# Optimization experiments

Measured on AMD Instinct MI355X. Metric: run time of the kernel, lower is better.

Reference implementation:

```python
import jax, jax.numpy as jnp
import numpy as np


def setup_inputs() -> dict:
    key = jax.random.key(0)
    ks = jax.random.split(key, 8)
    dim, E = 128, 8
    b, t, h, w = 2, 16, 64, 64
    scale = 1.0 / np.sqrt(dim)
    return {
        "x": jax.random.normal(ks[0], (b, dim, t, h, w), jnp.float32),
        "gate_w": jax.random.normal(ks[1], (dim, E), jnp.float32) * scale,
        "gate_b": jax.random.normal(ks[2], (E,), jnp.float32) * 0.01,
        "W1": jax.random.normal(ks[3], (E, dim, dim), jnp.float32) * scale,
        "b1": jax.random.normal(ks[4], (E, dim), jnp.float32) * 0.01,
        "alpha": jnp.full((E,), 0.25, jnp.float32),  # PReLU default init
        "W2": jax.random.normal(ks[5], (E, dim, dim), jnp.float32) * scale,
        "b2": jax.random.normal(ks[6], (E, dim), jnp.float32) * 0.01,
        "top_k": 2,
    }


def reference(x, gate_w, gate_b, W1, b1, alpha, W2, b2, top_k):
    b, c, t, h, w = x.shape
    E = gate_w.shape[1]
    # tokens: [N, c] with N = b*t*h*w (matches permute(0,2,3,4,1).reshape(-1,c))
    xf = jnp.transpose(x, (0, 2, 3, 4, 1)).reshape(-1, c)
    N = xf.shape[0]
    logits = xf @ gate_w + gate_b                      # [N, E]
    vals, idx = jax.lax.top_k(logits, top_k)           # [N, K]
    probs = jax.nn.softmax(vals, axis=1)               # softmax over selected logits
    # scatter combine weights to dense [N, E] (zero for unselected experts)
    combine = jnp.zeros((N, E), xf.dtype).at[jnp.arange(N)[:, None], idx].add(probs)
    # expert MLP (1x1x1 conv == per-token linear), scalar PReLU per expert
    h1 = jnp.einsum('nc,eoc->eno', xf, W1) + b1[:, None, :]          # [E, N, c]
    h1 = jnp.maximum(h1, 0) + alpha[:, None, None] * jnp.minimum(h1, 0)
    h2 = jnp.einsum('eno,epo->enp', h1, W2) + b2[:, None, :]         # [E, N, c]
    out = jnp.einsum('ne,enc->nc', combine, h2)                      # weighted combine
    out = jnp.transpose(out.reshape(b, t, h, w, c), (0, 4, 1, 2, 3))
    return out + x
```

## Files before the change

kernel.cpp:

```cpp
#include <hip/hip_runtime.h>

typedef float f32x4  __attribute__((ext_vector_type(4)));
typedef float f32x16 __attribute__((ext_vector_type(16)));
typedef __bf16 bf16x8 __attribute__((ext_vector_type(8)));

#define SPAT 65536
#define CH   128
#define NE   8

#define SLOT(i)  ((i) * 32768)
#define B1_OFF   65536
#define B2T_OFF  69632
#define AL_OFF   73728
#define LDS_BYTES 73760

static __device__ __forceinline__ unsigned short bf(float f) {
    __bf16 h = (__bf16)f; return __builtin_bit_cast(unsigned short, h);
}
static __device__ __forceinline__ unsigned pk2(float a, float b) {
    return (unsigned)bf(a) | ((unsigned)bf(b) << 16);
}

typedef const __attribute__((address_space(1))) void* as1cp;
typedef __attribute__((address_space(3))) void* as3p;
static __device__ __forceinline__ void gload16(const void* g, void* l) {
    __builtin_amdgcn_global_load_lds((as1cp)g, (as3p)l, 16, 0, 0);
}

__global__ void conv_w(const float* __restrict__ W1, const float* __restrict__ W2,
                       unsigned char* __restrict__ wimg) {
    const int gid = blockIdx.x * 256 + threadIdx.x;
    const int mat = gid >> 14;
    const int e   = (gid >> 11) & 7;
    const int r   = (gid >> 4) & 127;
    const int p   = gid & 15;
    if (mat == 0) {
        const int sg = p ^ (r & 15);
        const int n = 4 * (r >> 5) + ((r >> 3) & 3);
        const int src_row = (n >> 1) * 16 + ((r >> 2) & 1) * 8 + (n & 1) * 4 + (r & 3);
        const float* s = W1 + (e * 16384 + src_row * 128 + sg * 8);
        uint4 pk;
        pk.x = pk2(s[0], s[1]); pk.y = pk2(s[2], s[3]);
        pk.z = pk2(s[4], s[5]); pk.w = pk2(s[6], s[7]);
        *(uint4*)(wimg + e * 32768 + r * 256 + p * 16) = pk;
    } else {
        const float* s = W2 + (e * 16384 + r * 128 + p * 8);
        uint4 pk;
        pk.x = pk2(s[0], s[1]); pk.y = pk2(s[2], s[3]);
        pk.z = pk2(s[4], s[5]); pk.w = pk2(s[6], s[7]);
        *(uint4*)(wimg + 262144 + e * 32768
                  + ((((p >> 1) * 4 + (r >> 5)) << 10) + ((p & 1) << 9) + (r & 31) * 16)) = pk;
    }
}

static __device__ __forceinline__ void stage_w32(const unsigned char* __restrict__ src,
                                                 unsigned char* dst, int t) {
    const int off = t * 16;
    gload16(src + off,          dst + off);
    gload16(src + 8192  + off,  dst + 8192  + off);
    gload16(src + 16384 + off,  dst + 16384 + off);
    gload16(src + 24576 + off,  dst + 24576 + off);
}

__global__ __launch_bounds__(512) __attribute__((amdgpu_waves_per_eu(2, 2)))
void moe_main(const float* __restrict__ x,  const float* __restrict__ gw,
              const float* __restrict__ gb, const float* __restrict__ b1,
              const float* __restrict__ alpha, const float* __restrict__ b2,
              const unsigned char* __restrict__ wimg, float* __restrict__ out)
{
    __shared__ __align__(16) unsigned char smem[LDS_BYTES];
    const int t = threadIdx.x, lane = t & 63, w = t >> 6, blk = blockIdx.x;
    const int ltok = lane & 31, hi = lane >> 5, l15 = lane & 15;
    const size_t xbase = (size_t)(blk >> 8) * (size_t)(CH * SPAT) + (size_t)((blk & 255) << 8);
    const int m = w * 32 + ltok;
    const int wlane = (hi << 9) + ltok * 16;

    stage_w32(wimg, smem + SLOT(0), t);

    if (t < 256) ((f32x4*)(smem + B1_OFF))[t] = ((const f32x4*)b1)[t];
    if (t < 128) {
        uint4 pkv, z4 = {0u, 0u, 0u, 0u};
        pkv.x = pk2(b2[0 * 128 + t], b2[1 * 128 + t]);
        pkv.y = pk2(b2[2 * 128 + t], b2[3 * 128 + t]);
        pkv.z = pk2(b2[4 * 128 + t], b2[5 * 128 + t]);
        pkv.w = pk2(b2[6 * 128 + t], b2[7 * 128 + t]);
        *(uint4*)(smem + B2T_OFF + t * 32)      = pkv;
        *(uint4*)(smem + B2T_OFF + t * 32 + 16) = z4;
    } else if (t >= 128 && t < 136) {
        ((float*)(smem + AL_OFF))[t - 128] = alpha[t - 128];
    }

    f32x4 plo = {0.f,0.f,0.f,0.f}, phi = {0.f,0.f,0.f,0.f};
    uint4 xb[8];
    #pragma unroll
    for (int kc = 0; kc < 8; ++kc) {
        const int c0 = kc * 16 + hi * 8;
        float v8[8];
        #pragma unroll
        for (int j = 0; j < 8; ++j) v8[j] = x[xbase + (size_t)(c0 + j) * SPAT + m];
        #pragma unroll
        for (int j = 0; j < 8; ++j) {
            const f32x4 g0 = *(const f32x4*)(gw + (c0 + j) * NE);
            const f32x4 g1 = *(const f32x4*)(gw + (c0 + j) * NE + 4);
            plo += v8[j] * g0; phi += v8[j] * g1;
        }
        xb[kc].x = pk2(v8[0], v8[1]); xb[kc].y = pk2(v8[2], v8[3]);
        xb[kc].z = pk2(v8[4], v8[5]); xb[kc].w = pk2(v8[6], v8[7]);
    }
    #pragma unroll
    for (int i2 = 0; i2 < 4; ++i2) {
        plo[i2] += __shfl_xor(plo[i2], 32, 64);
        phi[i2] += __shfl_xor(phi[i2], 32, 64);
    }
    int i0, i1; float q0, q1; uint4 cbw;
    {
        float lg[8];
        #pragma unroll
        for (int e2 = 0; e2 < 4; ++e2) { lg[e2] = plo[e2] + gb[e2]; lg[4 + e2] = phi[e2] + gb[4 + e2]; }
        i0 = 0; float v0 = lg[0];
        #pragma unroll
        for (int e2 = 1; e2 < 8; ++e2) if (lg[e2] > v0) { v0 = lg[e2]; i0 = e2; }
        i1 = -1; float v1 = -3.4e38f;
        #pragma unroll
        for (int e2 = 0; e2 < 8; ++e2) if (e2 != i0 && lg[e2] > v1) { v1 = lg[e2]; i1 = e2; }
        const float d = expf(v1 - v0);
        q0 = 1.f / (1.f + d);
        q1 = d   / (1.f + d);
        float cb[8];
        #pragma unroll
        for (int e2 = 0; e2 < 8; ++e2) cb[e2] = (e2 == i0) ? q0 : ((e2 == i1) ? q1 : 0.f);
        cbw.x = pk2(cb[0], cb[1]); cbw.y = pk2(cb[2], cb[3]);
        cbw.z = pk2(cb[4], cb[5]); cbw.w = pk2(cb[6], cb[7]);
    }
    __syncthreads();

    f32x16 acc[4] = {};

    #pragma unroll 1
    for (int e = 0; e < NE; ++e) {
        const int cur = e & 1;
        if (e < 7) stage_w32(wimg + (e + 1) * 32768, smem + SLOT(cur ^ 1), t);
        const unsigned char* WA  = smem + SLOT(cur);
        const unsigned char* W2g = wimg + 262144 + e * 32768;
        const float alph = ((const float*)(smem + AL_OFF))[e];
        const float ce = (i0 == e) ? q0 : ((i1 == e) ? q1 : 0.f);

        #pragma unroll 1
        for (int g = 0; g < 4; ++g) {
            uint4 a1[8];
            #pragma unroll
            for (int kc = 0; kc < 8; ++kc)
                a1[kc] = *(const uint4*)(WA + (g * 32 + ltok) * 256
                                          + (((kc * 2 + hi) ^ l15) * 16));
            f32x16 h0 = {}, h1 = {};
            #pragma unroll
            for (int kc = 0; kc < 4; ++kc) {
                h0 = __builtin_amdgcn_mfma_f32_32x32x16_bf16(
                        __builtin_bit_cast(bf16x8, a1[2 * kc]),
                        __builtin_bit_cast(bf16x8, xb[2 * kc]), h0, 0, 0, 0);
                h1 = __builtin_amdgcn_mfma_f32_32x32x16_bf16(
                        __builtin_bit_cast(bf16x8, a1[2 * kc + 1]),
                        __builtin_bit_cast(bf16x8, xb[2 * kc + 1]), h1, 0, 0, 0);
            }
            uint4 pa2[2];
            #pragma unroll
            for (int q = 0; q < 4; ++q) {
                const int n = 4 * g + q, kt2 = n >> 1, half = n & 1;
                const int obase = kt2 * 16 + hi * 8 + half * 4;
                const f32x4 b1v = *(const f32x4*)(smem + B1_OFF + e * 512 + obase * 4);
                float hv[4];
                #pragma unroll
                for (int i = 0; i < 4; ++i) {
                    float z = h0[q * 4 + i] + h1[q * 4 + i] + b1v[i];
                    z = (z > 0.f) ? z : alph * z;
                    hv[i] = z * ce;
                }
                ((unsigned*)&pa2[q >> 1])[half * 2]     = pk2(hv[0], hv[1]);
                ((unsigned*)&pa2[q >> 1])[half * 2 + 1] = pk2(hv[2], hv[3]);
            }
            #pragma unroll
            for (int dk = 0; dk < 2; ++dk) {
                const int kt2 = 2 * g + dk;
                #pragma unroll
                for (int n2 = 0; n2 < 4; ++n2) {
                    const uint4 wf = *(const uint4*)(W2g + ((kt2 * 4 + n2) << 10) + wlane);
                    acc[n2] = __builtin_amdgcn_mfma_f32_32x32x16_bf16(
                            __builtin_bit_cast(bf16x8, pa2[dk]),
                            __builtin_bit_cast(bf16x8, wf), acc[n2], 0, 0, 0);
                }
            }
        }
        __syncthreads();
    }

    {
        const uint4 z4 = {0u, 0u, 0u, 0u};
        const uint4 aop = hi ? z4 : cbw;
        #pragma unroll
        for (int n2 = 0; n2 < 4; ++n2) {
            const uint4 bop = *(const uint4*)(smem + B2T_OFF + (n2 * 32 + ltok) * 32 + hi * 16);
            acc[n2] = __builtin_amdgcn_mfma_f32_32x32x16_bf16(
                    __builtin_bit_cast(bf16x8, aop),
                    __builtin_bit_cast(bf16x8, bop), acc[n2], 0, 0, 0);
        }
    }

    #pragma unroll
    for (int n2 = 0; n2 < 4; ++n2) {
        const int p = n2 * 32 + ltok;
        #pragma unroll
        for (int q = 0; q < 4; ++q) {
            const int tok0 = w * 32 + q * 8 + hi * 4;
            const size_t a = xbase + (size_t)p * SPAT + tok0;
            const f32x4 xv = *(const f32x4*)(x + a);
            f32x4 r;
            #pragma unroll
            for (int i = 0; i < 4; ++i) r[i] = acc[n2][q * 4 + i] + xv[i];
            *(f32x4*)(out + a) = r;
        }
    }
}

extern "C" void kernel_launch(void* const* d_in, const int* in_sizes, int n_in,
                              void* d_out, int out_size, void* d_ws, size_t ws_size,
                              hipStream_t stream) {
    const float* x  = (const float*)d_in[0];
    const float* gw = (const float*)d_in[1];
    const float* gb = (const float*)d_in[2];
    const float* W1 = (const float*)d_in[3];
    const float* b1 = (const float*)d_in[4];
    const float* al = (const float*)d_in[5];
    const float* W2 = (const float*)d_in[6];
    const float* b2 = (const float*)d_in[7];
    (void)in_sizes; (void)n_in; (void)out_size; (void)ws_size;
    unsigned char* wimg = (unsigned char*)d_ws;
    float* out = (float*)d_out;

    conv_w<<<dim3(128), dim3(256), 0, stream>>>(W1, W2, wimg);
    moe_main<<<dim3(512), dim3(512), 0, stream>>>(x, gw, gb, b1, al, b2, wimg, out);
}
```

Baseline: 122.1 us.

## Load W1 fragments from global into registers with double buffering, drop LDS staging

W1 is no longer staged into LDS through global_load_lds. It is repacked into the same MFMA-fragment layout as W2 and loaded straight from global (L2) into registers. The loads are software-pipelined one (expert, group) iteration ahead, with sched_barriers to keep the order, which removes the per-expert __syncthreads and LDS reads. LDS use drops from about 72 KB to about 8 KB. In exchange the kernel carries more VGPRs for the two prefetch buffers and the W2 fragments, and every wave now pulls its weights from L2 instead of sharing them through LDS.

```diff
diff --git a/kernel.cpp b/kernel.cpp
--- a/kernel.cpp
+++ b/kernel.cpp
@@ -8,23 +8,18 @@
 #define CH   128
 #define NE   8
 
-#define SLOT(i)  ((i) * 32768)
-#define B1_OFF   65536
-#define B2T_OFF  69632
-#define AL_OFF   73728
-#define LDS_BYTES 73760
+#define B1_OFF   0
+#define B2T_OFF  4096
+#define AL_OFF   8192
+#define LDS_BYTES 8224
+
+#define SB() __builtin_amdgcn_sched_barrier(0)
 
 static __device__ __forceinline__ unsigned short bf(float f) {
     __bf16 h = (__bf16)f; return __builtin_bit_cast(unsigned short, h);
 }
 static __device__ __forceinline__ unsigned pk2(float a, float b) {
     return (unsigned)bf(a) | ((unsigned)bf(b) << 16);
-}
-
-typedef const __attribute__((address_space(1))) void* as1cp;
-typedef __attribute__((address_space(3))) void* as3p;
-static __device__ __forceinline__ void gload16(const void* g, void* l) {
-    __builtin_amdgcn_global_load_lds((as1cp)g, (as3p)l, 16, 0, 0);
 }
 
 __global__ void conv_w(const float* __restrict__ W1, const float* __restrict__ W2,
@@ -34,32 +29,84 @@
     const int e   = (gid >> 11) & 7;
     const int r   = (gid >> 4) & 127;
     const int p   = gid & 15;
+    int src_row = r;
     if (mat == 0) {
-        const int sg = p ^ (r & 15);
         const int n = 4 * (r >> 5) + ((r >> 3) & 3);
-        const int src_row = (n >> 1) * 16 + ((r >> 2) & 1) * 8 + (n & 1) * 4 + (r & 3);
-        const float* s = W1 + (e * 16384 + src_row * 128 + sg * 8);
-        uint4 pk;
-        pk.x = pk2(s[0], s[1]); pk.y = pk2(s[2], s[3]);
-        pk.z = pk2(s[4], s[5]); pk.w = pk2(s[6], s[7]);
-        *(uint4*)(wimg + e * 32768 + r * 256 + p * 16) = pk;
-    } else {
-        const float* s = W2 + (e * 16384 + r * 128 + p * 8);
-        uint4 pk;
-        pk.x = pk2(s[0], s[1]); pk.y = pk2(s[2], s[3]);
-        pk.z = pk2(s[4], s[5]); pk.w = pk2(s[6], s[7]);
-        *(uint4*)(wimg + 262144 + e * 32768
-                  + ((((p >> 1) * 4 + (r >> 5)) << 10) + ((p & 1) << 9) + (r & 31) * 16)) = pk;
-    }
-}
-
-static __device__ __forceinline__ void stage_w32(const unsigned char* __restrict__ src,
-                                                 unsigned char* dst, int t) {
-    const int off = t * 16;
-    gload16(src + off,          dst + off);
-    gload16(src + 8192  + off,  dst + 8192  + off);
-    gload16(src + 16384 + off,  dst + 16384 + off);
-    gload16(src + 24576 + off,  dst + 24576 + off);
+        src_row = (n >> 1) * 16 + ((r >> 2) & 1) * 8 + (n & 1) * 4 + (r & 3);
+    }
+    const float* s = (mat ? W2 : W1) + (e * 16384 + src_row * 128 + p * 8);
+    uint4 pk;
+    pk.x = pk2(s[0], s[1]); pk.y = pk2(s[2], s[3]);
+    pk.z = pk2(s[4], s[5]); pk.w = pk2(s[6], s[7]);
+    *(uint4*)(wimg + mat * 262144 + e * 32768
+              + ((((p >> 1) * 4 + (r >> 5)) << 10) + ((p & 1) << 9) + (r & 31) * 16)) = pk;
+}
+
+static __device__ __forceinline__ void ld_a1g(uint4* buf, const unsigned char* __restrict__ base,
+                                              int g, int wlane) {
+    #pragma unroll
+    for (int kc = 0; kc < 8; ++kc)
+        buf[kc] = *(const uint4*)(base + ((kc * 4 + g) << 10) + wlane);
+}
+
+static __device__ __forceinline__ void body(
+        int it, uint4* cur, uint4* nxt,
+        const unsigned char* __restrict__ wimg, const unsigned char* smem,
+        int wlane, int hi, int i0, int i1, float q0, float q1,
+        const uint4* xb, f32x16* acc)
+{
+    const int e = it >> 2, g = it & 3;
+    const unsigned char* W2g = wimg + 262144 + e * 32768;
+
+    uint4 wfb[8];
+    #pragma unroll
+    for (int dk = 0; dk < 2; ++dk)
+        #pragma unroll
+        for (int n2 = 0; n2 < 4; ++n2)
+            wfb[dk * 4 + n2] = *(const uint4*)(W2g + (((2 * g + dk) * 4 + n2) << 10) + wlane);
+    SB();
+    if (it < 31) {
+        const int en = (it + 1) >> 2, gn = (it + 1) & 3;
+        ld_a1g(nxt, wimg + en * 32768, gn, wlane);
+    }
+    SB();
+
+    f32x16 h0 = {}, h1 = {};
+    #pragma unroll
+    for (int kc = 0; kc < 4; ++kc) {
+        h0 = __builtin_amdgcn_mfma_f32_32x32x16_bf16(
+                __builtin_bit_cast(bf16x8, cur[2 * kc]),
+                __builtin_bit_cast(bf16x8, xb[2 * kc]), h0, 0, 0, 0);
+        h1 = __builtin_amdgcn_mfma_f32_32x32x16_bf16(
+                __builtin_bit_cast(bf16x8, cur[2 * kc + 1]),
+                __builtin_bit_cast(bf16x8, xb[2 * kc + 1]), h1, 0, 0, 0);
+    }
+    const float alph = ((const float*)(smem + AL_OFF))[e];
+    const float ce = (i0 == e) ? q0 : ((i1 == e) ? q1 : 0.f);
+    uint4 pa2[2];
+    #pragma unroll
+    for (int q = 0; q < 4; ++q) {
+        const int n = 4 * g + q, kt2 = n >> 1, half = n & 1;
+        const int obase = kt2 * 16 + hi * 8 + half * 4;
+        const f32x4 b1v = *(const f32x4*)(smem + B1_OFF + e * 512 + obase * 4);
+        float hv[4];
+        #pragma unroll
+        for (int i = 0; i < 4; ++i) {
+            float z = h0[q * 4 + i] + h1[q * 4 + i] + b1v[i];
+            z = (z > 0.f) ? z : alph * z;
+            hv[i] = z * ce;
+        }
+        ((unsigned*)&pa2[q >> 1])[half * 2]     = pk2(hv[0], hv[1]);
+        ((unsigned*)&pa2[q >> 1])[half * 2 + 1] = pk2(hv[2], hv[3]);
+    }
+    SB();
+    #pragma unroll
+    for (int dk = 0; dk < 2; ++dk)
+        #pragma unroll
+        for (int n2 = 0; n2 < 4; ++n2)
+            acc[n2] = __builtin_amdgcn_mfma_f32_32x32x16_bf16(
+                    __builtin_bit_cast(bf16x8, pa2[dk]),
+                    __builtin_bit_cast(bf16x8, wfb[dk * 4 + n2]), acc[n2], 0, 0, 0);
 }
 
 __global__ __launch_bounds__(512) __attribute__((amdgpu_waves_per_eu(2, 2)))
@@ -70,12 +117,13 @@
 {
     __shared__ __align__(16) unsigned char smem[LDS_BYTES];
     const int t = threadIdx.x, lane = t & 63, w = t >> 6, blk = blockIdx.x;
-    const int ltok = lane & 31, hi = lane >> 5, l15 = lane & 15;
+    const int ltok = lane & 31, hi = lane >> 5;
     const size_t xbase = (size_t)(blk >> 8) * (size_t)(CH * SPAT) + (size_t)((blk & 255) << 8);
     const int m = w * 32 + ltok;
     const int wlane = (hi << 9) + ltok * 16;
 
-    stage_w32(wimg, smem + SLOT(0), t);
+    uint4 bufA[8], bufB[8];
+    ld_a1g(bufA, wimg, 0, wlane);
 
     if (t < 256) ((f32x4*)(smem + B1_OFF))[t] = ((const f32x4*)b1)[t];
     if (t < 128) {
@@ -137,60 +185,9 @@
     f32x16 acc[4] = {};
 
     #pragma unroll 1
-    for (int e = 0; e < NE; ++e) {
-        const int cur = e & 1;
-        if (e < 7) stage_w32(wimg + (e + 1) * 32768, smem + SLOT(cur ^ 1), t);
-        const unsigned char* WA  = smem + SLOT(cur);
-        const unsigned char* W2g = wimg + 262144 + e * 32768;
-        const float alph = ((const float*)(smem + AL_OFF))[e];
-        const float ce = (i0 == e) ? q0 : ((i1 == e) ? q1 : 0.f);
-
-        #pragma unroll 1
-        for (int g = 0; g < 4; ++g) {
-            uint4 a1[8];
-            #pragma unroll
-            for (int kc = 0; kc < 8; ++kc)
-                a1[kc] = *(const uint4*)(WA + (g * 32 + ltok) * 256
-                                          + (((kc * 2 + hi) ^ l15) * 16));
-            f32x16 h0 = {}, h1 = {};
-            #pragma unroll
-            for (int kc = 0; kc < 4; ++kc) {
-                h0 = __builtin_amdgcn_mfma_f32_32x32x16_bf16(
-                        __builtin_bit_cast(bf16x8, a1[2 * kc]),
-                        __builtin_bit_cast(bf16x8, xb[2 * kc]), h0, 0, 0, 0);
-                h1 = __builtin_amdgcn_mfma_f32_32x32x16_bf16(
-                        __builtin_bit_cast(bf16x8, a1[2 * kc + 1]),
-                        __builtin_bit_cast(bf16x8, xb[2 * kc + 1]), h1, 0, 0, 0);
-            }
-            uint4 pa2[2];
-            #pragma unroll
-            for (int q = 0; q < 4; ++q) {
-                const int n = 4 * g + q, kt2 = n >> 1, half = n & 1;
-                const int obase = kt2 * 16 + hi * 8 + half * 4;
-                const f32x4 b1v = *(const f32x4*)(smem + B1_OFF + e * 512 + obase * 4);
-                float hv[4];
-                #pragma unroll
-                for (int i = 0; i < 4; ++i) {
-                    float z = h0[q * 4 + i] + h1[q * 4 + i] + b1v[i];
-                    z = (z > 0.f) ? z : alph * z;
-                    hv[i] = z * ce;
-                }
-                ((unsigned*)&pa2[q >> 1])[half * 2]     = pk2(hv[0], hv[1]);
-                ((unsigned*)&pa2[q >> 1])[half * 2 + 1] = pk2(hv[2], hv[3]);
-            }
-            #pragma unroll
-            for (int dk = 0; dk < 2; ++dk) {
-                const int kt2 = 2 * g + dk;
-                #pragma unroll
-                for (int n2 = 0; n2 < 4; ++n2) {
-                    const uint4 wf = *(const uint4*)(W2g + ((kt2 * 4 + n2) << 10) + wlane);
-                    acc[n2] = __builtin_amdgcn_mfma_f32_32x32x16_bf16(
-                            __builtin_bit_cast(bf16x8, pa2[dk]),
-                            __builtin_bit_cast(bf16x8, wf), acc[n2], 0, 0, 0);
-                }
-            }
-        }
-        __syncthreads();
+    for (int itp = 0; itp < 16; ++itp) {
+        body(2 * itp,     bufA, bufB, wimg, smem, wlane, hi, i0, i1, q0, q1, xb, acc);
+        body(2 * itp + 1, bufB, bufA, wimg, smem, wlane, hi, i0, i1, q0, q1, xb, acc);
     }
 
     {
```

Result: slower. 134.2 us (+9.9%).

## Switch MoE kernel to 16x16 MFMA tiles with smaller blocks and single-buffered weights

Applied to the files above, without the earlier changes.

Reworks the fused MoE kernel around 16x16x32 bf16 MFMA instead of 32x32x16. Each block now handles 64 tokens with 256 threads, and 2048 blocks are launched. The W1 staging goes from a double buffer to a single LDS slot, and the next expert's weights are prefetched after the first GEMM behind an extra barrier. LDS use and accumulator registers drop so more waves fit per CU, and the weight-image layout in conv_w changes to match the new fragments. The cost is more blocks reloading weights, less overlap of the weight copy with compute, and an additional sync per expert.

```diff
diff --git a/kernel.cpp b/kernel.cpp
--- a/kernel.cpp
+++ b/kernel.cpp
@@ -1,18 +1,17 @@
 #include <hip/hip_runtime.h>
 
 typedef float f32x4  __attribute__((ext_vector_type(4)));
-typedef float f32x16 __attribute__((ext_vector_type(16)));
 typedef __bf16 bf16x8 __attribute__((ext_vector_type(8)));
 
 #define SPAT 65536
 #define CH   128
 #define NE   8
 
-#define SLOT(i)  ((i) * 32768)
-#define B1_OFF   65536
-#define B2T_OFF  69632
-#define AL_OFF   73728
-#define LDS_BYTES 73760
+#define SLOT_OFF 0
+#define B1_OFF   32768
+#define B2T_OFF  36864
+#define AL_OFF   38912
+#define LDS_BYTES 38944
 
 static __device__ __forceinline__ unsigned short bf(float f) {
     __bf16 h = (__bf16)f; return __builtin_bit_cast(unsigned short, h);
@@ -32,69 +31,65 @@
     const int gid = blockIdx.x * 256 + threadIdx.x;
     const int mat = gid >> 14;
     const int e   = (gid >> 11) & 7;
-    const int r   = (gid >> 4) & 127;
-    const int p   = gid & 15;
+    const int L   = (gid >> 6) & 31;
+    const int l   = gid & 63;
+    const int qk  = l >> 4;
+    const float* s;
     if (mat == 0) {
-        const int sg = p ^ (r & 15);
-        const int n = 4 * (r >> 5) + ((r >> 3) & 3);
-        const int src_row = (n >> 1) * 16 + ((r >> 2) & 1) * 8 + (n & 1) * 4 + (r & 3);
-        const float* s = W1 + (e * 16384 + src_row * 128 + sg * 8);
-        uint4 pk;
-        pk.x = pk2(s[0], s[1]); pk.y = pk2(s[2], s[3]);
-        pk.z = pk2(s[4], s[5]); pk.w = pk2(s[6], s[7]);
-        *(uint4*)(wimg + e * 32768 + r * 256 + p * 16) = pk;
+        const int g = L >> 2, b = L & 3, rt = l & 15;
+        const int P = ((g >> 1) << 5) + ((rt >> 2) << 3) + ((g & 1) << 2) + (rt & 3);
+        s = W1 + e * 16384 + P * 128 + (b << 5) + (qk << 3);
     } else {
-        const float* s = W2 + (e * 16384 + r * 128 + p * 8);
-        uint4 pk;
-        pk.x = pk2(s[0], s[1]); pk.y = pk2(s[2], s[3]);
-        pk.z = pk2(s[4], s[5]); pk.w = pk2(s[6], s[7]);
-        *(uint4*)(wimg + 262144 + e * 32768
-                  + ((((p >> 1) * 4 + (r >> 5)) << 10) + ((p & 1) << 9) + (r & 31) * 16)) = pk;
-    }
-}
-
-static __device__ __forceinline__ void stage_w32(const unsigned char* __restrict__ src,
-                                                 unsigned char* dst, int t) {
+        const int bb = L >> 3, pt = L & 7;
+        const int p = (pt << 4) + (l & 15);
+        s = W2 + e * 16384 + p * 128 + (bb << 5) + (qk << 3);
+    }
+    uint4 pk;
+    pk.x = pk2(s[0], s[1]); pk.y = pk2(s[2], s[3]);
+    pk.z = pk2(s[4], s[5]); pk.w = pk2(s[6], s[7]);
+    *(uint4*)(wimg + mat * 262144 + e * 32768 + L * 1024 + l * 16) = pk;
+}
+
+static __device__ __forceinline__ void stage_w(const unsigned char* __restrict__ src,
+                                               unsigned char* dst, int t) {
     const int off = t * 16;
-    gload16(src + off,          dst + off);
-    gload16(src + 8192  + off,  dst + 8192  + off);
-    gload16(src + 16384 + off,  dst + 16384 + off);
-    gload16(src + 24576 + off,  dst + 24576 + off);
-}
-
-__global__ __launch_bounds__(512) __attribute__((amdgpu_waves_per_eu(2, 2)))
+    #pragma unroll
+    for (int k = 0; k < 8; ++k)
+        gload16(src + k * 4096 + off, dst + k * 4096 + off);
+}
+
+__global__ __launch_bounds__(256) __attribute__((amdgpu_waves_per_eu(3, 8)))
 void moe_main(const float* __restrict__ x,  const float* __restrict__ gw,
               const float* __restrict__ gb, const float* __restrict__ b1,
               const float* __restrict__ alpha, const float* __restrict__ b2,
               const unsigned char* __restrict__ wimg, float* __restrict__ out)
 {
     __shared__ __align__(16) unsigned char smem[LDS_BYTES];
-    const int t = threadIdx.x, lane = t & 63, w = t >> 6, blk = blockIdx.x;
-    const int ltok = lane & 31, hi = lane >> 5, l15 = lane & 15;
-    const size_t xbase = (size_t)(blk >> 8) * (size_t)(CH * SPAT) + (size_t)((blk & 255) << 8);
-    const int m = w * 32 + ltok;
-    const int wlane = (hi << 9) + ltok * 16;
-
-    stage_w32(wimg, smem + SLOT(0), t);
+    const int t = threadIdx.x, l = t & 63, wv = t >> 6, blk = blockIdx.x;
+    const int tk = l & 15, q = l >> 4;
+    const size_t xbase = (size_t)(blk >> 10) * (size_t)(CH * SPAT) + (size_t)((blk & 1023) << 6);
+    const int m = wv * 16 + tk;
+    const int wl16 = l * 16;
+
+    stage_w(wimg, smem + SLOT_OFF, t);
 
     if (t < 256) ((f32x4*)(smem + B1_OFF))[t] = ((const f32x4*)b1)[t];
     if (t < 128) {
-        uint4 pkv, z4 = {0u, 0u, 0u, 0u};
-        pkv.x = pk2(b2[0 * 128 + t], b2[1 * 128 + t]);
-        pkv.y = pk2(b2[2 * 128 + t], b2[3 * 128 + t]);
-        pkv.z = pk2(b2[4 * 128 + t], b2[5 * 128 + t]);
-        pkv.w = pk2(b2[6 * 128 + t], b2[7 * 128 + t]);
-        *(uint4*)(smem + B2T_OFF + t * 32)      = pkv;
-        *(uint4*)(smem + B2T_OFF + t * 32 + 16) = z4;
+        uint4 p;
+        p.x = pk2(b2[0 * 128 + t], b2[1 * 128 + t]);
+        p.y = pk2(b2[2 * 128 + t], b2[3 * 128 + t]);
+        p.z = pk2(b2[4 * 128 + t], b2[5 * 128 + t]);
+        p.w = pk2(b2[6 * 128 + t], b2[7 * 128 + t]);
+        *(uint4*)(smem + B2T_OFF + t * 16) = p;
     } else if (t >= 128 && t < 136) {
         ((float*)(smem + AL_OFF))[t - 128] = alpha[t - 128];
     }
 
     f32x4 plo = {0.f,0.f,0.f,0.f}, phi = {0.f,0.f,0.f,0.f};
-    uint4 xb[8];
-    #pragma unroll
-    for (int kc = 0; kc < 8; ++kc) {
-        const int c0 = kc * 16 + hi * 8;
+    uint4 xb[4];
+    #pragma unroll
+    for (int b = 0; b < 4; ++b) {
+        const int c0 = b * 32 + q * 8;
         float v8[8];
         #pragma unroll
         for (int j = 0; j < 8; ++j) v8[j] = x[xbase + (size_t)(c0 + j) * SPAT + m];
@@ -104,11 +99,13 @@
             const f32x4 g1 = *(const f32x4*)(gw + (c0 + j) * NE + 4);
             plo += v8[j] * g0; phi += v8[j] * g1;
         }
-        xb[kc].x = pk2(v8[0], v8[1]); xb[kc].y = pk2(v8[2], v8[3]);
-        xb[kc].z = pk2(v8[4], v8[5]); xb[kc].w = pk2(v8[6], v8[7]);
+        xb[b].x = pk2(v8[0], v8[1]); xb[b].y = pk2(v8[2], v8[3]);
+        xb[b].z = pk2(v8[4], v8[5]); xb[b].w = pk2(v8[6], v8[7]);
     }
     #pragma unroll
     for (int i2 = 0; i2 < 4; ++i2) {
+        plo[i2] += __shfl_xor(plo[i2], 16, 64);
+        phi[i2] += __shfl_xor(phi[i2], 16, 64);
         plo[i2] += __shfl_xor(plo[i2], 32, 64);
         phi[i2] += __shfl_xor(phi[i2], 32, 64);
     }
@@ -134,90 +131,77 @@
     }
     __syncthreads();
 
-    f32x16 acc[4] = {};
+    f32x4 acc[8] = {};
 
     #pragma unroll 1
     for (int e = 0; e < NE; ++e) {
-        const int cur = e & 1;
-        if (e < 7) stage_w32(wimg + (e + 1) * 32768, smem + SLOT(cur ^ 1), t);
-        const unsigned char* WA  = smem + SLOT(cur);
-        const unsigned char* W2g = wimg + 262144 + e * 32768;
         const float alph = ((const float*)(smem + AL_OFF))[e];
         const float ce = (i0 == e) ? q0 : ((i1 == e) ? q1 : 0.f);
 
-        #pragma unroll 1
-        for (int g = 0; g < 4; ++g) {
-            uint4 a1[8];
-            #pragma unroll
-            for (int kc = 0; kc < 8; ++kc)
-                a1[kc] = *(const uint4*)(WA + (g * 32 + ltok) * 256
-                                          + (((kc * 2 + hi) ^ l15) * 16));
-            f32x16 h0 = {}, h1 = {};
-            #pragma unroll
-            for (int kc = 0; kc < 4; ++kc) {
-                h0 = __builtin_amdgcn_mfma_f32_32x32x16_bf16(
-                        __builtin_bit_cast(bf16x8, a1[2 * kc]),
-                        __builtin_bit_cast(bf16x8, xb[2 * kc]), h0, 0, 0, 0);
-                h1 = __builtin_amdgcn_mfma_f32_32x32x16_bf16(
-                        __builtin_bit_cast(bf16x8, a1[2 * kc + 1]),
-                        __builtin_bit_cast(bf16x8, xb[2 * kc + 1]), h1, 0, 0, 0);
+        uint4 pa[4];
+        #pragma unroll 2
+        for (int g = 0; g < 8; ++g) {
+            uint4 a1[4];
+            #pragma unroll
+            for (int b = 0; b < 4; ++b)
+                a1[b] = *(const uint4*)(smem + SLOT_OFF + (g * 4 + b) * 1024 + wl16);
+            f32x4 h = {0.f, 0.f, 0.f, 0.f};
+            #pragma unroll
+            for (int b = 0; b < 4; ++b)
+                h = __builtin_amdgcn_mfma_f32_16x16x32_bf16(
+                        __builtin_bit_cast(bf16x8, a1[b]),
+                        __builtin_bit_cast(bf16x8, xb[b]), h, 0, 0, 0);
+            const int ob = ((g >> 1) << 5) + (q << 3) + ((g & 1) << 2);
+            const f32x4 b1v = *(const f32x4*)(smem + B1_OFF + e * 512 + ob * 4);
+            float hv[4];
+            #pragma unroll
+            for (int i = 0; i < 4; ++i) {
+                float z = h[i] + b1v[i];
+                z = (z > 0.f) ? z : alph * z;
+                hv[i] = z * ce;
             }
-            uint4 pa2[2];
-            #pragma unroll
-            for (int q = 0; q < 4; ++q) {
-                const int n = 4 * g + q, kt2 = n >> 1, half = n & 1;
-                const int obase = kt2 * 16 + hi * 8 + half * 4;
-                const f32x4 b1v = *(const f32x4*)(smem + B1_OFF + e * 512 + obase * 4);
-                float hv[4];
-                #pragma unroll
-                for (int i = 0; i < 4; ++i) {
-                    float z = h0[q * 4 + i] + h1[q * 4 + i] + b1v[i];
-                    z = (z > 0.f) ? z : alph * z;
-                    hv[i] = z * ce;
-                }
-                ((unsigned*)&pa2[q >> 1])[half * 2]     = pk2(hv[0], hv[1]);
-                ((unsigned*)&pa2[q >> 1])[half * 2 + 1] = pk2(hv[2], hv[3]);
+            ((unsigned*)&pa[g >> 1])[(g & 1) * 2]     = pk2(hv[0], hv[1]);
+            ((unsigned*)&pa[g >> 1])[(g & 1) * 2 + 1] = pk2(hv[2], hv[3]);
+        }
+        __syncthreads();
+        if (e < 7) stage_w(wimg + (e + 1) * 32768, smem + SLOT_OFF, t);
+
+        const unsigned char* W2g = wimg + 262144 + e * 32768;
+        #pragma unroll 2
+        for (int b = 0; b < 4; ++b) {
+            #pragma unroll
+            for (int pt = 0; pt < 8; ++pt) {
+                const uint4 wf = *(const uint4*)(W2g + (b * 8 + pt) * 1024 + wl16);
+                acc[pt] = __builtin_amdgcn_mfma_f32_16x16x32_bf16(
+                        __builtin_bit_cast(bf16x8, pa[b]),
+                        __builtin_bit_cast(bf16x8, wf), acc[pt], 0, 0, 0);
             }
-            #pragma unroll
-            for (int dk = 0; dk < 2; ++dk) {
-                const int kt2 = 2 * g + dk;
-                #pragma unroll
-                for (int n2 = 0; n2 < 4; ++n2) {
-                    const uint4 wf = *(const uint4*)(W2g + ((kt2 * 4 + n2) << 10) + wlane);
-                    acc[n2] = __builtin_amdgcn_mfma_f32_32x32x16_bf16(
-                            __builtin_bit_cast(bf16x8, pa2[dk]),
-                            __builtin_bit_cast(bf16x8, wf), acc[n2], 0, 0, 0);
-                }
-            }
-        }
-        __syncthreads();
+        }
+        if (e < 7) __syncthreads();
     }
 
     {
         const uint4 z4 = {0u, 0u, 0u, 0u};
-        const uint4 aop = hi ? z4 : cbw;
-        #pragma unroll
-        for (int n2 = 0; n2 < 4; ++n2) {
-            const uint4 bop = *(const uint4*)(smem + B2T_OFF + (n2 * 32 + ltok) * 32 + hi * 16);
-            acc[n2] = __builtin_amdgcn_mfma_f32_32x32x16_bf16(
+        const uint4 aop = (q == 0) ? cbw : z4;
+        #pragma unroll
+        for (int pt = 0; pt < 8; ++pt) {
+            const uint4 bop = (q == 0)
+                ? *(const uint4*)(smem + B2T_OFF + (pt * 16 + tk) * 16) : z4;
+            acc[pt] = __builtin_amdgcn_mfma_f32_16x16x32_bf16(
                     __builtin_bit_cast(bf16x8, aop),
-                    __builtin_bit_cast(bf16x8, bop), acc[n2], 0, 0, 0);
-        }
-    }
-
-    #pragma unroll
-    for (int n2 = 0; n2 < 4; ++n2) {
-        const int p = n2 * 32 + ltok;
-        #pragma unroll
-        for (int q = 0; q < 4; ++q) {
-            const int tok0 = w * 32 + q * 8 + hi * 4;
-            const size_t a = xbase + (size_t)p * SPAT + tok0;
-            const f32x4 xv = *(const f32x4*)(x + a);
-            f32x4 r;
-            #pragma unroll
-            for (int i = 0; i < 4; ++i) r[i] = acc[n2][q * 4 + i] + xv[i];
-            *(f32x4*)(out + a) = r;
-        }
+                    __builtin_bit_cast(bf16x8, bop), acc[pt], 0, 0, 0);
+        }
+    }
+
+    #pragma unroll
+    for (int pt = 0; pt < 8; ++pt) {
+        const int p = pt * 16 + tk;
+        const size_t a = xbase + (size_t)p * SPAT + (wv * 16 + q * 4);
+        const f32x4 xv = *(const f32x4*)(x + a);
+        f32x4 r;
+        #pragma unroll
+        for (int i = 0; i < 4; ++i) r[i] = acc[pt][i] + xv[i];
+        *(f32x4*)(out + a) = r;
     }
 }
 
@@ -237,5 +221,5 @@
     float* out = (float*)d_out;
 
     conv_w<<<dim3(128), dim3(256), 0, stream>>>(W1, W2, wimg);
-    moe_main<<<dim3(512), dim3(512), 0, stream>>>(x, gw, gb, b1, al, b2, wimg, out);
-}
+    moe_main<<<dim3(2048), dim3(256), 0, stream>>>(x, gw, gb, b1, al, b2, wimg, out);
+}
```

New measurement: 179.9 us. 47.3% more time.
